# Optimization experiments

Hardware: AMD Instinct MI355X
Metric: run time of the kernel (lower is better)

Reference implementation:

```python
import jax, jax.numpy as jnp
import numpy as np

B, LT, D, N, H = 16, 512, 1024, 4096, 16
LN_EPS = 1e-5


def setup_inputs() -> dict:
    key = jax.random.key(0)
    ks = jax.random.split(key, 10)
    s = 0.02
    struct_token = jax.random.normal(ks[0], (N, D), dtype=jnp.float32)
    text_token = jax.random.normal(ks[1], (B, LT, D), dtype=jnp.float32)
    # contiguous, sorted segment ids: 256 struct tokens per batch element
    struct_batch = jnp.repeat(jnp.arange(B, dtype=jnp.int32), N // B)
    return {
        "struct_token": struct_token,
        "text_token": text_token,
        "in_proj_w": jax.random.normal(ks[2], (3 * D, D), dtype=jnp.float32) * s,
        "in_proj_b": jnp.zeros((3 * D,), jnp.float32),
        "attn_out_w": jax.random.normal(ks[3], (D, D), dtype=jnp.float32) * s,
        "attn_out_b": jnp.zeros((D,), jnp.float32),
        "ln_g": jnp.ones((D,), jnp.float32),
        "ln_b": jnp.zeros((D,), jnp.float32),
        "proj_w": jax.random.normal(ks[4], (D, D), dtype=jnp.float32) * s,
        "proj_b": jnp.zeros((D,), jnp.float32),
        "struct_batch": struct_batch,
        "L_max": N // B,
    }


def reference(struct_token, text_token, in_proj_w, in_proj_b, attn_out_w,
              attn_out_b, ln_g, ln_b, proj_w, proj_b, struct_batch, L_max):
    Bq = text_token.shape[0]
    Dm = struct_token.shape[-1]
    dh = Dm // H
    Ntok = struct_token.shape[0]

    # ---- ragged pad-pack (struct_batch is sorted/contiguous per segment) ----
    counts = jnp.bincount(struct_batch, length=Bq)                 # [B]
    starts = jnp.concatenate([jnp.zeros((1,), counts.dtype),
                              jnp.cumsum(counts)[:-1]])            # [B]
    pos = jnp.arange(Ntok) - starts[struct_batch]                  # [N] position in segment
    padded = jnp.zeros((Bq, L_max, Dm), struct_token.dtype)
    padded = padded.at[struct_batch, pos].set(struct_token)        # [B, Ls, D]

    # ---- nn.MultiheadAttention (batch_first): Q=padded, K=V=text ----
    wq, wk, wv = in_proj_w[:Dm], in_proj_w[Dm:2 * Dm], in_proj_w[2 * Dm:]
    bq, bk, bv = in_proj_b[:Dm], in_proj_b[Dm:2 * Dm], in_proj_b[2 * Dm:]
    q = (padded @ wq.T + bq).reshape(Bq, L_max, H, dh)
    k = (text_token @ wk.T + bk).reshape(Bq, -1, H, dh)
    v = (text_token @ wv.T + bv).reshape(Bq, -1, H, dh)
    scores = jnp.einsum('bqhd,bkhd->bhqk', q, k) / jnp.sqrt(jnp.float32(dh))
    attn = jax.nn.softmax(scores, axis=-1)
    ctx = jnp.einsum('bhqk,bkhd->bqhd', attn, v).reshape(Bq, L_max, Dm)
    fused = ctx @ attn_out_w.T + attn_out_b                        # [B, Ls, D]

    # ---- LayerNorm + output projection ----
    mu = fused.mean(-1, keepdims=True)
    var = fused.var(-1, keepdims=True)
    fused = (fused - mu) * jax.lax.rsqrt(var + LN_EPS) * ln_g + ln_b
    fused = fused @ proj_w.T + proj_b

    # ---- unpack valid tokens + scatter-mean over segments ----
    tok = fused[struct_batch, pos]                                 # [N, D]
    seg_sum = jax.ops.segment_sum(tok, struct_batch, num_segments=Bq)
    return seg_sum / jnp.maximum(counts, 1)[:, None].astype(seg_sum.dtype)
```

## Files before the change

kernel.cpp:

```cpp
#include <hip/hip_runtime.h>

constexpr int B  = 16;
constexpr int LT = 512;
constexpr int D  = 1024;
constexpr int N  = 4096;
constexpr int H  = 16;
constexpr int DH = D / H;
constexpr int LMAX = N / B;
constexpr float LN_EPS = 1e-5f;

typedef short  s16x8 __attribute__((ext_vector_type(8)));
typedef float  f32x4 __attribute__((ext_vector_type(4)));

__device__ __forceinline__ unsigned short f2bf(float x) {
    unsigned int u = __float_as_uint(x);
    unsigned int r = (u + 0x7fffu + ((u >> 16) & 1u)) >> 16;
    return (unsigned short)r;
}
__device__ __forceinline__ float bf2f(unsigned short u) {
    return __uint_as_float((unsigned int)u << 16);
}

__device__ __forceinline__ void load_lds16(const void* g, void* l) {
    __builtin_amdgcn_global_load_lds(
        (const __attribute__((address_space(1))) unsigned int*)g,
        (__attribute__((address_space(3))) unsigned int*)l, 16, 0, 0);
}

__global__ __launch_bounds__(256) void cast3_prep(
        const float* __restrict__ x0, unsigned short* __restrict__ y0, int n0,
        const float* __restrict__ x1, unsigned short* __restrict__ y1, int n1,
        const float* __restrict__ x2, unsigned short* __restrict__ y2, int n2,
        const int* __restrict__ sb, int* __restrict__ counts, int* __restrict__ starts,
        float* __restrict__ msum) {
    __shared__ int s_counts[B];
    int t = threadIdx.x;
    if (blockIdx.x == 6144) {
        if (t < B) s_counts[t] = 0;
        __syncthreads();
        for (int i = t; i < N; i += 256) atomicAdd(&s_counts[sb[i]], 1);
        __syncthreads();
        if (t == 0) {
            int run = 0;
            for (int b = 0; b < B; b++) { starts[b] = run; run += s_counts[b]; }
        }
        if (t < B) counts[t] = s_counts[t];
        return;
    }
    if (blockIdx.x == 6145) {
        float4 z = {0.f, 0.f, 0.f, 0.f};
#pragma unroll
        for (int c = 0; c < 16; c++)
            ((float4*)msum)[c * 256 + t] = z;
        return;
    }
    long long i = (long long)(blockIdx.x * 256 + t) * 8;
    const float* x; unsigned short* y;
    if (i < n0)                { x = x0 + i; y = y0 + i; }
    else if (i < (long long)n0 + n1) { long long j = i - n0; x = x1 + j; y = y1 + j; }
    else if (i < (long long)n0 + n1 + n2) { long long j = i - n0 - n1; x = x2 + j; y = y2 + j; }
    else return;
    float4 a = *(const float4*)x;
    float4 b = *(const float4*)(x + 4);
    ushort4 o1, o2;
    o1.x = f2bf(a.x); o1.y = f2bf(a.y); o1.z = f2bf(a.z); o1.w = f2bf(a.w);
    o2.x = f2bf(b.x); o2.y = f2bf(b.y); o2.z = f2bf(b.z); o2.w = f2bf(b.w);
    *(ushort4*)y = o1;
    *(ushort4*)(y + 4) = o2;
}

__global__ void scatter_full(const float* __restrict__ st,
                             const int* __restrict__ counts,
                             const int* __restrict__ starts,
                             unsigned short* __restrict__ padded) {
    int p = blockIdx.x, b = blockIdx.y;
    int d = threadIdx.x * 4;
    size_t off = ((size_t)(b * LMAX + p)) * D + d;
    ushort4 o = {0, 0, 0, 0};
    if (p < counts[b]) {
        float4 v = *(const float4*)&st[(size_t)(starts[b] + p) * D + d];
        o.x = f2bf(v.x); o.y = f2bf(v.y); o.z = f2bf(v.z); o.w = f2bf(v.w);
    }
    *(ushort4*)&padded[off] = o;
}

template<typename Epi>
__device__ __forceinline__ void gemm32(const unsigned short* __restrict__ A,
                                       const unsigned short* __restrict__ W,
                                       int K, int kbeg, int kend, int m0, int n0,
                                       unsigned short* __restrict__ As,
                                       unsigned short* __restrict__ Bs,
                                       Epi&& epi) {
    const int tid  = threadIdx.x;
    const int lane = tid & 63;
    const int wid  = tid >> 6;
    const int wr   = wid >> 1;
    const int wc   = wid & 1;
    const int fm   = lane & 15;
    const int quad = lane >> 4;
    const int NK   = (kend - kbeg) >> 5;

    f32x4 acc[4][4];
#pragma unroll
    for (int i = 0; i < 4; i++)
#pragma unroll
        for (int j = 0; j < 4; j++) acc[i][j] = (f32x4){0.f, 0.f, 0.f, 0.f};

    const int rA0 = tid >> 2,          sA0 = (tid & 3) ^ ((tid >> 3) & 3);
    const int cA1 = tid + 512;
    const int rA1 = cA1 >> 2,          sA1 = (cA1 & 3) ^ ((cA1 >> 3) & 3);
    const unsigned short* gA0 = A + (size_t)(m0 + rA0) * K + kbeg + sA0 * 8;
    const unsigned short* gA1 = A + (size_t)(m0 + rA1) * K + kbeg + sA1 * 8;
    const unsigned short* gB  = W + (size_t)(n0 + rA0) * K + kbeg + sA0 * 8;
    unsigned short* lA0 = As + (size_t)tid * 8;
    unsigned short* lA1 = As + (size_t)(tid + 512) * 8;
    unsigned short* lB  = Bs + (size_t)tid * 8;

    const int sl8 = (quad ^ ((fm >> 1) & 3)) * 8;
    int offA[4], offB[4];
#pragma unroll
    for (int i = 0; i < 4; i++) offA[i] = (wr * 64 + i * 16 + fm) * 32 + sl8;
#pragma unroll
    for (int j = 0; j < 4; j++) offB[j] = (wc * 64 + j * 16 + fm) * 32 + sl8;

    load_lds16(gA0, lA0);
    load_lds16(gA1, lA1);
    load_lds16(gB , lB );

    for (int s = 0; s < NK; s++) {
        const int ab = (s & 1) << 13;
        const int bb = (s & 1) << 12;
        asm volatile("s_barrier" ::: "memory");
        if (s + 1 < NK) {
            const int go = (s + 1) << 5;
            const int ab2 = ((s + 1) & 1) << 13;
            const int bb2 = ((s + 1) & 1) << 12;
            load_lds16(gA0 + go, lA0 + ab2);
            load_lds16(gA1 + go, lA1 + ab2);
            load_lds16(gB  + go, lB  + bb2);
            asm volatile("s_waitcnt vmcnt(3)" ::: "memory");
        } else {
            asm volatile("s_waitcnt vmcnt(0)" ::: "memory");
        }
        asm volatile("s_barrier" ::: "memory");

        s16x8 af[4], bfv[4];
#pragma unroll
        for (int i = 0; i < 4; i++) af[i] = *(const s16x8*)&As[ab + offA[i]];
#pragma unroll
        for (int j = 0; j < 4; j++) bfv[j] = *(const s16x8*)&Bs[bb + offB[j]];

        __builtin_amdgcn_s_setprio(1);
#pragma unroll
        for (int i = 0; i < 4; i++)
#pragma unroll
            for (int j = 0; j < 4; j++)
                acc[i][j] = __builtin_amdgcn_mfma_f32_16x16x32_bf16(af[i], bfv[j], acc[i][j], 0, 0, 0);
        __builtin_amdgcn_s_setprio(0);
    }

    const int fr = quad * 4;
#pragma unroll
    for (int i = 0; i < 4; i++)
#pragma unroll
        for (int j = 0; j < 4; j++) {
            int row = m0 + wr * 64 + i * 16 + fr;
            int col = n0 + wc * 64 + j * 16 + fm;
#pragma unroll
            for (int r = 0; r < 4; r++)
                epi(row + r, col, acc[i][j][r]);
        }
}

template<typename Epi>
__device__ __forceinline__ void gemm128(const unsigned short* __restrict__ A,
                                        const unsigned short* __restrict__ W,
                                        int K, int kbeg, int kend, int m0, int n0,
                                        unsigned short* __restrict__ As,
                                        unsigned short* __restrict__ Bs,
                                        Epi&& epi) {
    const int tid  = threadIdx.x;
    const int lane = tid & 63;
    const int wid  = tid >> 6;
    const int wr   = wid >> 1;
    const int wc   = wid & 1;
    const int fm   = lane & 15;
    const int quad = lane >> 4;
    const int NK   = (kend - kbeg) >> 5;

    f32x4 acc[4][4];
#pragma unroll
    for (int i = 0; i < 4; i++)
#pragma unroll
        for (int j = 0; j < 4; j++) acc[i][j] = (f32x4){0.f, 0.f, 0.f, 0.f};

    const int r0 = tid >> 2, s0 = (tid & 3) ^ ((tid >> 3) & 3);
    const unsigned short* gA0 = A + (size_t)(m0 + r0) * K + kbeg + s0 * 8;
    const unsigned short* gA1 = gA0 + (size_t)64 * K;
    const unsigned short* gB0 = W + (size_t)(n0 + r0) * K + kbeg + s0 * 8;
    const unsigned short* gB1 = gB0 + (size_t)64 * K;
    unsigned short* lA0 = As + (size_t)tid * 8;
    unsigned short* lA1 = As + (size_t)(tid + 256) * 8;
    unsigned short* lB0 = Bs + (size_t)tid * 8;
    unsigned short* lB1 = Bs + (size_t)(tid + 256) * 8;

    const int sl8 = (quad ^ ((fm >> 1) & 3)) * 8;
    int offA[4], offB[4];
#pragma unroll
    for (int i = 0; i < 4; i++) offA[i] = (wr * 64 + i * 16 + fm) * 32 + sl8;
#pragma unroll
    for (int j = 0; j < 4; j++) offB[j] = (wc * 64 + j * 16 + fm) * 32 + sl8;

    load_lds16(gA0, lA0);
    load_lds16(gA1, lA1);
    load_lds16(gB0, lB0);
    load_lds16(gB1, lB1);

    for (int s = 0; s < NK; s++) {
        const int ab = (s & 1) << 12;
        const int bb = (s & 1) << 12;
        asm volatile("s_barrier" ::: "memory");
        if (s + 1 < NK) {
            const int go = (s + 1) << 5;
            const int nb = ((s + 1) & 1) << 12;
            load_lds16(gA0 + go, lA0 + nb);
            load_lds16(gA1 + go, lA1 + nb);
            load_lds16(gB0 + go, lB0 + nb);
            load_lds16(gB1 + go, lB1 + nb);
            asm volatile("s_waitcnt vmcnt(4)" ::: "memory");
        } else {
            asm volatile("s_waitcnt vmcnt(0)" ::: "memory");
        }
        asm volatile("s_barrier" ::: "memory");

        s16x8 af[4], bfv[4];
#pragma unroll
        for (int i = 0; i < 4; i++) af[i] = *(const s16x8*)&As[ab + offA[i]];
#pragma unroll
        for (int j = 0; j < 4; j++) bfv[j] = *(const s16x8*)&Bs[bb + offB[j]];

        __builtin_amdgcn_s_setprio(1);
#pragma unroll
        for (int i = 0; i < 4; i++)
#pragma unroll
            for (int j = 0; j < 4; j++)
                acc[i][j] = __builtin_amdgcn_mfma_f32_16x16x32_bf16(af[i], bfv[j], acc[i][j], 0, 0, 0);
        __builtin_amdgcn_s_setprio(0);
    }

    const int fr = quad * 4;
#pragma unroll
    for (int i = 0; i < 4; i++)
#pragma unroll
        for (int j = 0; j < 4; j++) {
            int row = m0 + wr * 64 + i * 16 + fr;
            int col = n0 + wc * 64 + j * 16 + fm;
#pragma unroll
            for (int r = 0; r < 4; r++)
                epi(row + r, col, acc[i][j][r]);
        }
}

__global__ __launch_bounds__(512, 4) void qkv_fused(const unsigned short* __restrict__ padded,
                                                    const unsigned short* __restrict__ text,
                                                    const unsigned short* __restrict__ wqkv,
                                                    const float* __restrict__ bqkv,
                                                    unsigned short* __restrict__ qpack,
                                                    unsigned short* __restrict__ kpack,
                                                    unsigned short* __restrict__ vpack) {
    __shared__ __align__(16) unsigned short As[2 * 8192];
    __shared__ __align__(16) unsigned short Bs[2 * 4096];
    int orig = blockIdx.x;
    int id = (orig & 7) * 80 + (orig >> 3);
    if (id < 128) {
        int mt = id >> 3, nt = id & 7;
        gemm32(padded, wqkv, D, 0, D, mt * 256, nt * 128, As, Bs,
            [&](int mm, int col, float v) {
                float val = v + bqkv[col];
                int b = mm >> 8, q = mm & 255;
                int h = col >> 6, d = col & 63;
                qpack[(size_t)(b * H + h) * 16384 + (d >> 3) * 2048 + q * 8 + (d & 7)] = f2bf(val);
            });
    } else if (id < 384) {
        int f = id - 128;
        int mt = f >> 3, nt = f & 7;
        gemm32(text, wqkv + (size_t)D * D, D, 0, D, mt * 256, nt * 128, As, Bs,
            [&](int mm, int col, float v) {
                float val = v + bqkv[D + col];
                int b = mm >> 9, key = mm & 511;
                int h = col >> 6, d = col & 63;
                kpack[(size_t)(b * H + h) * 32768 + (d >> 3) * 4096 + key * 8 + (d & 7)] = f2bf(val);
            });
    } else {
        int f = id - 384;
        int mt = f >> 6, nt = f & 63;
        gemm32(wqkv + 2 * (size_t)D * D, text, D, 0, D, mt * 256, nt * 128, As, Bs,
            [&](int mm, int col, float v) {
                float val = v + bqkv[2 * D + mm];
                int h = mm >> 6, d = mm & 63;
                int b = col >> 9, key = col & 511;
                vpack[(size_t)(b * H + h) * 32768 + (key >> 3) * 512 + d * 8 + (key & 7)] = f2bf(val);
            });
    }
}

__global__ __launch_bounds__(256, 4) void gemm_bf2(const unsigned short* __restrict__ A,
                                                   const unsigned short* __restrict__ W,
                                                   unsigned short* __restrict__ C0,
                                                   unsigned short* __restrict__ C1,
                                                   int Nn, int K) {
    __shared__ __align__(16) unsigned short As[2 * 4096];
    __shared__ __align__(16) unsigned short Bs[2 * 4096];
    int orig = blockIdx.x;
    int id = (orig & 7) * 64 + (orig >> 3);
    int kh = id >> 8;
    int f  = id & 255;
    int mt = f >> 3, nt = f & 7;
    unsigned short* C = kh ? C1 : C0;
    gemm128(A, W, K, kh * 512, (kh + 1) * 512, mt * 128, nt * 128, As, Bs,
        [&](int mm, int col, float v) {
            C[(size_t)mm * Nn + col] = f2bf(v);
        });
}

constexpr int PKW = 72;

__global__ __launch_bounds__(512) void attn_mfma(const unsigned short* __restrict__ qpack,
                                                 const unsigned short* __restrict__ kpack,
                                                 const unsigned short* __restrict__ vpack,
                                                 unsigned short* __restrict__ ctx) {
    __shared__ __align__(16) unsigned short KV[2][16384];
    __shared__ __align__(16) unsigned short Ps[8 * 16 * PKW];

    const int tid = threadIdx.x;
    const int lane = tid & 63;
    const int wv = tid >> 6;
    const int fm = lane & 15;
    const int quad = lane >> 4;
    const int h = blockIdx.x, b = blockIdx.y, half = blockIdx.z;
    const int q0 = half * 128 + wv * 16;

    const unsigned short* qp = qpack + (size_t)(b * H + h) * 16384;
    const unsigned short* kp = kpack + (size_t)(b * H + h) * 32768;
    const unsigned short* vp = vpack + (size_t)(b * H + h) * 32768;

    const s16x8 aq0 = *(const s16x8*)&qp[quad * 2048 + (q0 + fm) * 8];
    const s16x8 aq1 = *(const s16x8*)&qp[(4 + quad) * 2048 + (q0 + fm) * 8];

#pragma unroll
    for (int kc = 0; kc < 2; kc++)
#pragma unroll
        for (int it = 0; it < 4; it++) {
            int f = it * 512 + tid;
            load_lds16(kp + (f >> 8) * 4096 + kc * 2048 + (f & 255) * 8, &KV[kc][f * 8]);
        }

    f32x4 sc[32];

    asm volatile("s_waitcnt vmcnt(4)" ::: "memory");
    __builtin_amdgcn_s_barrier();
    __builtin_amdgcn_s_setprio(1);
#pragma unroll
    for (int t = 0; t < 16; t++) {
        s16x8 bk0 = *(const s16x8*)&KV[0][quad * 2048 + (t * 16 + fm) * 8];
        s16x8 bk1 = *(const s16x8*)&KV[0][(4 + quad) * 2048 + (t * 16 + fm) * 8];
        f32x4 a = (f32x4){0.f, 0.f, 0.f, 0.f};
        a = __builtin_amdgcn_mfma_f32_16x16x32_bf16(aq0, bk0, a, 0, 0, 0);
        a = __builtin_amdgcn_mfma_f32_16x16x32_bf16(aq1, bk1, a, 0, 0, 0);
        sc[t] = a;
    }
    __builtin_amdgcn_s_setprio(0);

    asm volatile("s_waitcnt vmcnt(0)" ::: "memory");
    __builtin_amdgcn_s_barrier();
    __builtin_amdgcn_s_setprio(1);
#pragma unroll
    for (int t = 0; t < 16; t++) {
        s16x8 bk0 = *(const s16x8*)&KV[1][quad * 2048 + (t * 16 + fm) * 8];
        s16x8 bk1 = *(const s16x8*)&KV[1][(4 + quad) * 2048 + (t * 16 + fm) * 8];
        f32x4 a = (f32x4){0.f, 0.f, 0.f, 0.f};
        a = __builtin_amdgcn_mfma_f32_16x16x32_bf16(aq0, bk0, a, 0, 0, 0);
        a = __builtin_amdgcn_mfma_f32_16x16x32_bf16(aq1, bk1, a, 0, 0, 0);
        sc[16 + t] = a;
    }
    __builtin_amdgcn_s_setprio(0);

    asm volatile("s_waitcnt lgkmcnt(0)" ::: "memory");
    __builtin_amdgcn_s_barrier();

#pragma unroll
    for (int vc = 0; vc < 2; vc++)
#pragma unroll
        for (int it = 0; it < 4; it++) {
            int f = it * 512 + tid;
            load_lds16(vp + vc * 16384 + f * 8, &KV[vc][f * 8]);
        }

    const float scale = 0.125f;
    float mx[4], l[4], inv[4];
#pragma unroll
    for (int r = 0; r < 4; r++) {
        float m = sc[0][r];
#pragma unroll
        for (int t = 1; t < 32; t++) m = fmaxf(m, sc[t][r]);
        mx[r] = m;
    }
#pragma unroll
    for (int o = 1; o < 16; o <<= 1)
#pragma unroll
        for (int r = 0; r < 4; r++) mx[r] = fmaxf(mx[r], __shfl_xor(mx[r], o));
#pragma unroll
    for (int r = 0; r < 4; r++) l[r] = 0.f;
#pragma unroll
    for (int t = 0; t < 32; t++)
#pragma unroll
        for (int r = 0; r < 4; r++) {
            float e = __expf((sc[t][r] - mx[r]) * scale);
            sc[t][r] = e;
            l[r] += e;
        }
#pragma unroll
    for (int o = 1; o < 16; o <<= 1)
#pragma unroll
        for (int r = 0; r < 4; r++) l[r] += __shfl_xor(l[r], o);
#pragma unroll
    for (int r = 0; r < 4; r++) inv[r] = 1.f / l[r];

    f32x4 co[4];
#pragma unroll
    for (int n = 0; n < 4; n++) co[n] = (f32x4){0.f, 0.f, 0.f, 0.f};
    unsigned short* Pw = Ps + wv * (16 * PKW);

    asm volatile("s_waitcnt vmcnt(4)" ::: "memory");
    __builtin_amdgcn_s_barrier();

    for (int vc = 0; vc < 2; vc++) {
        if (vc == 1) {
            asm volatile("s_waitcnt vmcnt(0)" ::: "memory");
            __builtin_amdgcn_s_barrier();
        }
        for (int cs = 0; cs < 4; cs++) {
            int c = vc * 4 + cs;
#pragma unroll
            for (int tt = 0; tt < 4; tt++)
#pragma unroll
                for (int r = 0; r < 4; r++)
                    Pw[(quad * 4 + r) * PKW + tt * 16 + fm] = f2bf(sc[c * 4 + tt][r]);
            __builtin_amdgcn_s_setprio(1);
#pragma unroll
            for (int s = 0; s < 2; s++) {
                s16x8 ap = *(const s16x8*)&Pw[fm * PKW + s * 32 + quad * 8];
#pragma unroll
                for (int n = 0; n < 4; n++) {
                    s16x8 bv = *(const s16x8*)&KV[vc][(cs * 8 + s * 4 + quad) * 512 + (n * 16 + fm) * 8];
                    co[n] = __builtin_amdgcn_mfma_f32_16x16x32_bf16(ap, bv, co[n], 0, 0, 0);
                }
            }
            __builtin_amdgcn_s_setprio(0);
        }
    }

    const size_t obase = (size_t)(b * LMAX + q0) * D + h * DH;
#pragma unroll
    for (int n = 0; n < 4; n++)
#pragma unroll
        for (int r = 0; r < 4; r++)
            ctx[obase + (size_t)(quad * 4 + r) * D + n * 16 + fm] = f2bf(co[n][r] * inv[r]);
}

__global__ __launch_bounds__(256) void lnmean_kernel(const unsigned short* __restrict__ f1a,
                                                     const unsigned short* __restrict__ f1b,
                                                     const float* __restrict__ bo,
                                                     const float* __restrict__ g,
                                                     const float* __restrict__ bb,
                                                     const int* __restrict__ counts,
                                                     float* __restrict__ msum) {
    int b = blockIdx.x;
    int t = threadIdx.x;
    int wv = t >> 6, lane = t & 63;
    int cnt = counts[b];
    int s0 = blockIdx.y * 32 + wv * 8;
    int s1 = min(cnt, s0 + 8);

    float4 gg[4], bv[4], bo4[4];
#pragma unroll
    for (int c = 0; c < 4; c++) {
        gg[c]  = *(const float4*)&g[c * 256 + lane * 4];
        bv[c]  = *(const float4*)&bb[c * 256 + lane * 4];
        bo4[c] = *(const float4*)&bo[c * 256 + lane * 4];
    }
    float4 acc[4];
#pragma unroll
    for (int c = 0; c < 4; c++) acc[c] = (float4){0.f, 0.f, 0.f, 0.f};

    for (int s = s0; s < s1; s++) {
        size_t rbase = ((size_t)(b * LMAX + s)) * D;
        float4 v[4];
        float sm = 0.f, ss = 0.f;
#pragma unroll
        for (int c = 0; c < 4; c++) {
            ushort4 ua = *(const ushort4*)&f1a[rbase + c * 256 + lane * 4];
            ushort4 ub = *(const ushort4*)&f1b[rbase + c * 256 + lane * 4];
            v[c].x = bf2f(ua.x) + bf2f(ub.x) + bo4[c].x;
            v[c].y = bf2f(ua.y) + bf2f(ub.y) + bo4[c].y;
            v[c].z = bf2f(ua.z) + bf2f(ub.z) + bo4[c].z;
            v[c].w = bf2f(ua.w) + bf2f(ub.w) + bo4[c].w;
            sm += v[c].x + v[c].y + v[c].z + v[c].w;
            ss += v[c].x * v[c].x + v[c].y * v[c].y + v[c].z * v[c].z + v[c].w * v[c].w;
        }
#pragma unroll
        for (int o = 32; o; o >>= 1) { sm += __shfl_xor(sm, o); ss += __shfl_xor(ss, o); }
        float mu = sm * (1.f / D);
        float var = ss * (1.f / D) - mu * mu;
        float r = rsqrtf(var + LN_EPS);
#pragma unroll
        for (int c = 0; c < 4; c++) {
            acc[c].x += (v[c].x - mu) * r * gg[c].x + bv[c].x;
            acc[c].y += (v[c].y - mu) * r * gg[c].y + bv[c].y;
            acc[c].z += (v[c].z - mu) * r * gg[c].z + bv[c].z;
            acc[c].w += (v[c].w - mu) * r * gg[c].w + bv[c].w;
        }
    }
    float inv = 1.f / (float)max(cnt, 1);
#pragma unroll
    for (int c = 0; c < 4; c++) {
        int base = b * D + c * 256 + lane * 4;
        atomicAdd(&msum[base + 0], acc[c].x * inv);
        atomicAdd(&msum[base + 1], acc[c].y * inv);
        atomicAdd(&msum[base + 2], acc[c].z * inv);
        atomicAdd(&msum[base + 3], acc[c].w * inv);
    }
}

__global__ __launch_bounds__(256) void tproj_kernel(const float* __restrict__ msum,
                                                    const float* __restrict__ W,
                                                    const float* __restrict__ bias,
                                                    float* __restrict__ out) {
    int lane = threadIdx.x & 63;
    int n = blockIdx.x * 4 + (threadIdx.x >> 6);
    float4 wr[4];
#pragma unroll
    for (int i = 0; i < 4; i++)
        wr[i] = *(const float4*)&W[(size_t)n * D + i * 256 + lane * 4];
    float bn = bias[n];
    for (int b = 0; b < B; b++) {
        float s = 0.f;
#pragma unroll
        for (int i = 0; i < 4; i++) {
            float4 m4 = *(const float4*)&msum[(size_t)b * D + i * 256 + lane * 4];
            s += m4.x * wr[i].x + m4.y * wr[i].y + m4.z * wr[i].z + m4.w * wr[i].w;
        }
#pragma unroll
        for (int o = 32; o; o >>= 1) s += __shfl_xor(s, o);
        if (lane == 0) out[(size_t)b * D + n] = s + bn;
    }
}

extern "C" void kernel_launch(void* const* d_in, const int* in_sizes, int n_in,
                              void* d_out, int out_size, void* d_ws, size_t ws_size,
                              hipStream_t stream) {
    const float* struct_token = (const float*)d_in[0];
    const float* text_token   = (const float*)d_in[1];
    const float* in_proj_w    = (const float*)d_in[2];
    const float* in_proj_b    = (const float*)d_in[3];
    const float* attn_out_w   = (const float*)d_in[4];
    const float* attn_out_b   = (const float*)d_in[5];
    const float* ln_g         = (const float*)d_in[6];
    const float* ln_b         = (const float*)d_in[7];
    const float* proj_w       = (const float*)d_in[8];
    const float* proj_b       = (const float*)d_in[9];
    const int*   sb           = (const int*)d_in[10];
    float* out = (float*)d_out;

    const size_t MQ  = (size_t)B * LMAX;
    const size_t MKV = (size_t)B * LT;

    char* p = (char*)d_ws;
    unsigned short* padded_b = (unsigned short*)p;  p += MQ * D * 2;
    unsigned short* text_b   = (unsigned short*)p;  p += MKV * D * 2;
    unsigned short* wqkv_b   = (unsigned short*)p;  p += (size_t)3 * D * D * 2;
    unsigned short* wattn_b  = (unsigned short*)p;  p += (size_t)D * D * 2;
    unsigned short* qpack    = (unsigned short*)p;  p += MQ * D * 2;
    unsigned short* kpack    = (unsigned short*)p;  p += MKV * D * 2;
    unsigned short* vpack    = (unsigned short*)p;  p += MKV * D * 2;
    unsigned short* ctx_b    = (unsigned short*)p;  p += MQ * D * 2;
    unsigned short* f1a      = (unsigned short*)p;  p += MQ * D * 2;
    unsigned short* f1b      = (unsigned short*)p;  p += MQ * D * 2;
    float* msum = (float*)p;  p += (size_t)B * D * 4;
    int* counts = (int*)p;  p += B * 4;
    int* starts = (int*)p;  p += B * 4;

    cast3_prep<<<6146, 256, 0, stream>>>(
        text_token, text_b, (int)(MKV * D),
        in_proj_w,  wqkv_b, 3 * D * D,
        attn_out_w, wattn_b, D * D,
        sb, counts, starts, msum);

    scatter_full<<<dim3(LMAX, B), 256, 0, stream>>>(struct_token, counts, starts, padded_b);

    qkv_fused<<<640, 512, 0, stream>>>(padded_b, text_b, wqkv_b, in_proj_b,
                                       qpack, kpack, vpack);

    attn_mfma<<<dim3(H, B, 2), 512, 0, stream>>>(qpack, kpack, vpack, ctx_b);

    gemm_bf2<<<512, 256, 0, stream>>>(ctx_b, wattn_b, f1a, f1b, D, D);

    lnmean_kernel<<<dim3(B, 8), 256, 0, stream>>>(f1a, f1b, attn_out_b, ln_g, ln_b, counts, msum);

    tproj_kernel<<<256, 256, 0, stream>>>(msum, proj_w, proj_b, out);
}
```

Before: 253.8 us.

## Stream attention with online softmax over 128-key chunks and triple-buffered K/V

Rewrites the attention kernel as a flash-style online softmax over four 128-key chunks instead of holding all 512 scores in registers. K and V chunks rotate through a three-slot LDS ring (48KB instead of 64KB), and the next chunk is prefetched while the current one is computed. Launch bounds now request 4 blocks per CU. Both changes aim to cut register and LDS pressure so more waves fit per CU. The cost is extra rescaling work per chunk and more barriers.

```diff
diff --git a/kernel.cpp b/kernel.cpp
--- a/kernel.cpp
+++ b/kernel.cpp
@@ -325,11 +325,11 @@
 
 constexpr int PKW = 72;
 
-__global__ __launch_bounds__(512) void attn_mfma(const unsigned short* __restrict__ qpack,
-                                                 const unsigned short* __restrict__ kpack,
-                                                 const unsigned short* __restrict__ vpack,
-                                                 unsigned short* __restrict__ ctx) {
-    __shared__ __align__(16) unsigned short KV[2][16384];
+__global__ __launch_bounds__(512, 4) void attn_mfma(const unsigned short* __restrict__ qpack,
+                                                    const unsigned short* __restrict__ kpack,
+                                                    const unsigned short* __restrict__ vpack,
+                                                    unsigned short* __restrict__ ctx) {
+    __shared__ __align__(16) unsigned short KV[3][8192];
     __shared__ __align__(16) unsigned short Ps[8 * 16 * PKW];
 
     const int tid = threadIdx.x;
@@ -347,118 +347,130 @@
     const s16x8 aq0 = *(const s16x8*)&qp[quad * 2048 + (q0 + fm) * 8];
     const s16x8 aq1 = *(const s16x8*)&qp[(4 + quad) * 2048 + (q0 + fm) * 8];
 
-#pragma unroll
-    for (int kc = 0; kc < 2; kc++)
-#pragma unroll
-        for (int it = 0; it < 4; it++) {
+    auto stageK = [&](int c, int bfi) {
+#pragma unroll
+        for (int it = 0; it < 2; it++) {
             int f = it * 512 + tid;
-            load_lds16(kp + (f >> 8) * 4096 + kc * 2048 + (f & 255) * 8, &KV[kc][f * 8]);
-        }
-
-    f32x4 sc[32];
-
-    asm volatile("s_waitcnt vmcnt(4)" ::: "memory");
-    __builtin_amdgcn_s_barrier();
-    __builtin_amdgcn_s_setprio(1);
-#pragma unroll
-    for (int t = 0; t < 16; t++) {
-        s16x8 bk0 = *(const s16x8*)&KV[0][quad * 2048 + (t * 16 + fm) * 8];
-        s16x8 bk1 = *(const s16x8*)&KV[0][(4 + quad) * 2048 + (t * 16 + fm) * 8];
-        f32x4 a = (f32x4){0.f, 0.f, 0.f, 0.f};
-        a = __builtin_amdgcn_mfma_f32_16x16x32_bf16(aq0, bk0, a, 0, 0, 0);
-        a = __builtin_amdgcn_mfma_f32_16x16x32_bf16(aq1, bk1, a, 0, 0, 0);
-        sc[t] = a;
-    }
-    __builtin_amdgcn_s_setprio(0);
-
-    asm volatile("s_waitcnt vmcnt(0)" ::: "memory");
-    __builtin_amdgcn_s_barrier();
-    __builtin_amdgcn_s_setprio(1);
-#pragma unroll
-    for (int t = 0; t < 16; t++) {
-        s16x8 bk0 = *(const s16x8*)&KV[1][quad * 2048 + (t * 16 + fm) * 8];
-        s16x8 bk1 = *(const s16x8*)&KV[1][(4 + quad) * 2048 + (t * 16 + fm) * 8];
-        f32x4 a = (f32x4){0.f, 0.f, 0.f, 0.f};
-        a = __builtin_amdgcn_mfma_f32_16x16x32_bf16(aq0, bk0, a, 0, 0, 0);
-        a = __builtin_amdgcn_mfma_f32_16x16x32_bf16(aq1, bk1, a, 0, 0, 0);
-        sc[16 + t] = a;
-    }
-    __builtin_amdgcn_s_setprio(0);
-
-    asm volatile("s_waitcnt lgkmcnt(0)" ::: "memory");
-    __builtin_amdgcn_s_barrier();
-
-#pragma unroll
-    for (int vc = 0; vc < 2; vc++)
-#pragma unroll
-        for (int it = 0; it < 4; it++) {
+            load_lds16(kp + (f >> 7) * 4096 + c * 1024 + (f & 127) * 8, &KV[bfi][f * 8]);
+        }
+    };
+    auto stageV = [&](int c, int bfi) {
+#pragma unroll
+        for (int it = 0; it < 2; it++) {
             int f = it * 512 + tid;
-            load_lds16(vp + vc * 16384 + f * 8, &KV[vc][f * 8]);
-        }
+            load_lds16(vp + c * 8192 + f * 8, &KV[bfi][f * 8]);
+        }
+    };
 
     const float scale = 0.125f;
-    float mx[4], l[4], inv[4];
-#pragma unroll
-    for (int r = 0; r < 4; r++) {
-        float m = sc[0][r];
-#pragma unroll
-        for (int t = 1; t < 32; t++) m = fmaxf(m, sc[t][r]);
-        mx[r] = m;
-    }
-#pragma unroll
-    for (int o = 1; o < 16; o <<= 1)
-#pragma unroll
-        for (int r = 0; r < 4; r++) mx[r] = fmaxf(mx[r], __shfl_xor(mx[r], o));
-#pragma unroll
-    for (int r = 0; r < 4; r++) l[r] = 0.f;
-#pragma unroll
-    for (int t = 0; t < 32; t++)
+    f32x4 co[4];
+#pragma unroll
+    for (int n = 0; n < 4; n++) co[n] = (f32x4){0.f, 0.f, 0.f, 0.f};
+    float m[4], l[4];
+#pragma unroll
+    for (int r = 0; r < 4; r++) { m[r] = -1e30f; l[r] = 0.f; }
+
+    unsigned short* Pw = Ps + wv * (16 * PKW);
+
+    stageK(0, 0);
+    stageV(0, 1);
+
+#pragma unroll
+    for (int c = 0; c < 4; c++) {
+        const int kb = (2 * c) % 3;
+        const int vb = (2 * c + 1) % 3;
+
+        asm volatile("s_waitcnt vmcnt(2)" ::: "memory");
+        __builtin_amdgcn_s_barrier();
+
+        f32x4 sc[8];
+        __builtin_amdgcn_s_setprio(1);
+#pragma unroll
+        for (int t = 0; t < 8; t++) {
+            s16x8 bk0 = *(const s16x8*)&KV[kb][quad * 1024 + (t * 16 + fm) * 8];
+            s16x8 bk1 = *(const s16x8*)&KV[kb][(4 + quad) * 1024 + (t * 16 + fm) * 8];
+            f32x4 a = (f32x4){0.f, 0.f, 0.f, 0.f};
+            a = __builtin_amdgcn_mfma_f32_16x16x32_bf16(aq0, bk0, a, 0, 0, 0);
+            a = __builtin_amdgcn_mfma_f32_16x16x32_bf16(aq1, bk1, a, 0, 0, 0);
+            sc[t] = a;
+        }
+        __builtin_amdgcn_s_setprio(0);
+
+        asm volatile("s_waitcnt lgkmcnt(0)" ::: "memory");
+        __builtin_amdgcn_s_barrier();
+        if (c < 3) stageK(c + 1, (2 * c + 2) % 3);
+
+        float cm[4];
 #pragma unroll
         for (int r = 0; r < 4; r++) {
-            float e = __expf((sc[t][r] - mx[r]) * scale);
-            sc[t][r] = e;
-            l[r] += e;
-        }
-#pragma unroll
-    for (int o = 1; o < 16; o <<= 1)
-#pragma unroll
-        for (int r = 0; r < 4; r++) l[r] += __shfl_xor(l[r], o);
-#pragma unroll
-    for (int r = 0; r < 4; r++) inv[r] = 1.f / l[r];
-
-    f32x4 co[4];
-#pragma unroll
-    for (int n = 0; n < 4; n++) co[n] = (f32x4){0.f, 0.f, 0.f, 0.f};
-    unsigned short* Pw = Ps + wv * (16 * PKW);
-
-    asm volatile("s_waitcnt vmcnt(4)" ::: "memory");
-    __builtin_amdgcn_s_barrier();
-
-    for (int vc = 0; vc < 2; vc++) {
-        if (vc == 1) {
-            asm volatile("s_waitcnt vmcnt(0)" ::: "memory");
-            __builtin_amdgcn_s_barrier();
-        }
-        for (int cs = 0; cs < 4; cs++) {
-            int c = vc * 4 + cs;
+            float mm = sc[0][r];
+#pragma unroll
+            for (int t = 1; t < 8; t++) mm = fmaxf(mm, sc[t][r]);
+            cm[r] = mm;
+        }
+#pragma unroll
+        for (int o = 1; o < 16; o <<= 1)
+#pragma unroll
+            for (int r = 0; r < 4; r++) cm[r] = fmaxf(cm[r], __shfl_xor(cm[r], o));
+        float al[4];
+#pragma unroll
+        for (int r = 0; r < 4; r++) {
+            float mn = fmaxf(m[r], cm[r]);
+            al[r] = __expf((m[r] - mn) * scale);
+            m[r] = mn;
+        }
+        float ls[4] = {0.f, 0.f, 0.f, 0.f};
+#pragma unroll
+        for (int t = 0; t < 8; t++)
+#pragma unroll
+            for (int r = 0; r < 4; r++) {
+                float e = __expf((sc[t][r] - m[r]) * scale);
+                sc[t][r] = e;
+                ls[r] += e;
+            }
+#pragma unroll
+        for (int r = 0; r < 4; r++) l[r] = l[r] * al[r] + ls[r];
+#pragma unroll
+        for (int n = 0; n < 4; n++)
+#pragma unroll
+            for (int r = 0; r < 4; r++) co[n][r] *= al[r];
+
+        if (c < 3) asm volatile("s_waitcnt vmcnt(2)" ::: "memory");
+        else       asm volatile("s_waitcnt vmcnt(0)" ::: "memory");
+        __builtin_amdgcn_s_barrier();
+
+#pragma unroll
+        for (int cs = 0; cs < 2; cs++) {
 #pragma unroll
             for (int tt = 0; tt < 4; tt++)
 #pragma unroll
                 for (int r = 0; r < 4; r++)
-                    Pw[(quad * 4 + r) * PKW + tt * 16 + fm] = f2bf(sc[c * 4 + tt][r]);
+                    Pw[(quad * 4 + r) * PKW + tt * 16 + fm] = f2bf(sc[cs * 4 + tt][r]);
             __builtin_amdgcn_s_setprio(1);
 #pragma unroll
             for (int s = 0; s < 2; s++) {
                 s16x8 ap = *(const s16x8*)&Pw[fm * PKW + s * 32 + quad * 8];
 #pragma unroll
                 for (int n = 0; n < 4; n++) {
-                    s16x8 bv = *(const s16x8*)&KV[vc][(cs * 8 + s * 4 + quad) * 512 + (n * 16 + fm) * 8];
+                    s16x8 bv = *(const s16x8*)&KV[vb][(cs * 8 + s * 4 + quad) * 512 + (n * 16 + fm) * 8];
                     co[n] = __builtin_amdgcn_mfma_f32_16x16x32_bf16(ap, bv, co[n], 0, 0, 0);
                 }
             }
             __builtin_amdgcn_s_setprio(0);
         }
-    }
+
+        asm volatile("s_waitcnt lgkmcnt(0)" ::: "memory");
+        __builtin_amdgcn_s_barrier();
+        if (c < 3) stageV(c + 1, (2 * c + 3) % 3);
+    }
+
+    float inv[4];
+#pragma unroll
+    for (int o = 1; o < 16; o <<= 1)
+#pragma unroll
+        for (int r = 0; r < 4; r++) l[r] += __shfl_xor(l[r], o);
+#pragma unroll
+    for (int r = 0; r < 4; r++) inv[r] = 1.f / l[r];
 
     const size_t obase = (size_t)(b * LMAX + q0) * D + h * DH;
 #pragma unroll
```

New measurement: 282.2 us. +11.2%, slower.

## Retile QKV GEMM to 128x128 tiles with K-step 64 and 256 threads

Applied to the files above, without the earlier changes.

The fused QKV projection kernel moves from 256x128 output tiles with 512 threads and a K-step of 32 to 128x128 tiles with 256 threads and a K-step of 64. Grid size doubles to 1280 blocks. The LDS swizzle is changed to an 8-way XOR layout, and each stage issues 8 async loads per thread with a matching vmcnt wait. The goal is fewer barriers per unit of MFMA work and better load balance across CUs. In exchange, each tile reuses less data, so global traffic per FLOP rises, and LDS grows to 64KB per block.

```diff
diff --git a/kernel.cpp b/kernel.cpp
--- a/kernel.cpp
+++ b/kernel.cpp
@@ -85,12 +85,12 @@
 }
 
 template<typename Epi>
-__device__ __forceinline__ void gemm32(const unsigned short* __restrict__ A,
-                                       const unsigned short* __restrict__ W,
-                                       int K, int kbeg, int kend, int m0, int n0,
-                                       unsigned short* __restrict__ As,
-                                       unsigned short* __restrict__ Bs,
-                                       Epi&& epi) {
+__device__ __forceinline__ void gemm128k64(const unsigned short* __restrict__ A,
+                                           const unsigned short* __restrict__ W,
+                                           int K, int kbeg, int kend, int m0, int n0,
+                                           unsigned short* __restrict__ As,
+                                           unsigned short* __restrict__ Bs,
+                                           Epi&& epi) {
     const int tid  = threadIdx.x;
     const int lane = tid & 63;
     const int wid  = tid >> 6;
@@ -98,7 +98,7 @@
     const int wc   = wid & 1;
     const int fm   = lane & 15;
     const int quad = lane >> 4;
-    const int NK   = (kend - kbeg) >> 5;
+    const int NK   = (kend - kbeg) >> 6;
 
     f32x4 acc[4][4];
 #pragma unroll
@@ -106,56 +106,73 @@
 #pragma unroll
         for (int j = 0; j < 4; j++) acc[i][j] = (f32x4){0.f, 0.f, 0.f, 0.f};
 
-    const int rA0 = tid >> 2,          sA0 = (tid & 3) ^ ((tid >> 3) & 3);
-    const int cA1 = tid + 512;
-    const int rA1 = cA1 >> 2,          sA1 = (cA1 & 3) ^ ((cA1 >> 3) & 3);
-    const unsigned short* gA0 = A + (size_t)(m0 + rA0) * K + kbeg + sA0 * 8;
-    const unsigned short* gA1 = A + (size_t)(m0 + rA1) * K + kbeg + sA1 * 8;
-    const unsigned short* gB  = W + (size_t)(n0 + rA0) * K + kbeg + sA0 * 8;
-    unsigned short* lA0 = As + (size_t)tid * 8;
-    unsigned short* lA1 = As + (size_t)(tid + 512) * 8;
-    unsigned short* lB  = Bs + (size_t)tid * 8;
-
-    const int sl8 = (quad ^ ((fm >> 1) & 3)) * 8;
-    int offA[4], offB[4];
-#pragma unroll
-    for (int i = 0; i < 4; i++) offA[i] = (wr * 64 + i * 16 + fm) * 32 + sl8;
-#pragma unroll
-    for (int j = 0; j < 4; j++) offB[j] = (wc * 64 + j * 16 + fm) * 32 + sl8;
-
-    load_lds16(gA0, lA0);
-    load_lds16(gA1, lA1);
-    load_lds16(gB , lB );
+    int rows[4], go8[4];
+#pragma unroll
+    for (int k = 0; k < 4; k++) {
+        int ci = tid + k * 256;
+        rows[k] = ci >> 3;
+        go8[k]  = ((ci & 7) ^ ((ci >> 3) & 7)) * 8;
+    }
+    const unsigned short* gA[4];
+    const unsigned short* gB[4];
+#pragma unroll
+    for (int k = 0; k < 4; k++) {
+        gA[k] = A + (size_t)(m0 + rows[k]) * K + kbeg + go8[k];
+        gB[k] = W + (size_t)(n0 + rows[k]) * K + kbeg + go8[k];
+    }
+
+    auto stage = [&](int s) {
+        const int go = s << 6;
+        unsigned short* Ad = As + (s & 1) * 8192;
+        unsigned short* Bd = Bs + (s & 1) * 8192;
+#pragma unroll
+        for (int k = 0; k < 4; k++)
+            load_lds16(gA[k] + go, Ad + (size_t)(tid + k * 256) * 8);
+#pragma unroll
+        for (int k = 0; k < 4; k++)
+            load_lds16(gB[k] + go, Bd + (size_t)(tid + k * 256) * 8);
+    };
+
+    int offA[4][2], offB[4][2];
+#pragma unroll
+    for (int kk = 0; kk < 2; kk++) {
+        const int sl8 = ((kk * 4 + quad) ^ (fm & 7)) * 8;
+#pragma unroll
+        for (int i = 0; i < 4; i++) offA[i][kk] = (wr * 64 + i * 16 + fm) * 64 + sl8;
+#pragma unroll
+        for (int j = 0; j < 4; j++) offB[j][kk] = (wc * 64 + j * 16 + fm) * 64 + sl8;
+    }
+
+    stage(0);
 
     for (int s = 0; s < NK; s++) {
         const int ab = (s & 1) << 13;
-        const int bb = (s & 1) << 12;
         asm volatile("s_barrier" ::: "memory");
         if (s + 1 < NK) {
-            const int go = (s + 1) << 5;
-            const int ab2 = ((s + 1) & 1) << 13;
-            const int bb2 = ((s + 1) & 1) << 12;
-            load_lds16(gA0 + go, lA0 + ab2);
-            load_lds16(gA1 + go, lA1 + ab2);
-            load_lds16(gB  + go, lB  + bb2);
-            asm volatile("s_waitcnt vmcnt(3)" ::: "memory");
+            stage(s + 1);
+            asm volatile("s_waitcnt vmcnt(8)" ::: "memory");
         } else {
             asm volatile("s_waitcnt vmcnt(0)" ::: "memory");
         }
         asm volatile("s_barrier" ::: "memory");
 
-        s16x8 af[4], bfv[4];
-#pragma unroll
-        for (int i = 0; i < 4; i++) af[i] = *(const s16x8*)&As[ab + offA[i]];
-#pragma unroll
-        for (int j = 0; j < 4; j++) bfv[j] = *(const s16x8*)&Bs[bb + offB[j]];
+        s16x8 af[4][2], bfv[4][2];
+#pragma unroll
+        for (int kk = 0; kk < 2; kk++) {
+#pragma unroll
+            for (int i = 0; i < 4; i++) af[i][kk]  = *(const s16x8*)&As[ab + offA[i][kk]];
+#pragma unroll
+            for (int j = 0; j < 4; j++) bfv[j][kk] = *(const s16x8*)&Bs[ab + offB[j][kk]];
+        }
 
         __builtin_amdgcn_s_setprio(1);
 #pragma unroll
-        for (int i = 0; i < 4; i++)
-#pragma unroll
-            for (int j = 0; j < 4; j++)
-                acc[i][j] = __builtin_amdgcn_mfma_f32_16x16x32_bf16(af[i], bfv[j], acc[i][j], 0, 0, 0);
+        for (int kk = 0; kk < 2; kk++)
+#pragma unroll
+            for (int i = 0; i < 4; i++)
+#pragma unroll
+                for (int j = 0; j < 4; j++)
+                    acc[i][j] = __builtin_amdgcn_mfma_f32_16x16x32_bf16(af[i][kk], bfv[j][kk], acc[i][j], 0, 0, 0);
         __builtin_amdgcn_s_setprio(0);
     }
 
@@ -261,7 +278,7 @@
         }
 }
 
-__global__ __launch_bounds__(512, 4) void qkv_fused(const unsigned short* __restrict__ padded,
+__global__ __launch_bounds__(256, 2) void qkv_fused(const unsigned short* __restrict__ padded,
                                                     const unsigned short* __restrict__ text,
                                                     const unsigned short* __restrict__ wqkv,
                                                     const float* __restrict__ bqkv,
@@ -269,22 +286,22 @@
                                                     unsigned short* __restrict__ kpack,
                                                     unsigned short* __restrict__ vpack) {
     __shared__ __align__(16) unsigned short As[2 * 8192];
-    __shared__ __align__(16) unsigned short Bs[2 * 4096];
+    __shared__ __align__(16) unsigned short Bs[2 * 8192];
     int orig = blockIdx.x;
-    int id = (orig & 7) * 80 + (orig >> 3);
-    if (id < 128) {
+    int id = (orig & 7) * 160 + (orig >> 3);
+    if (id < 256) {
         int mt = id >> 3, nt = id & 7;
-        gemm32(padded, wqkv, D, 0, D, mt * 256, nt * 128, As, Bs,
+        gemm128k64(padded, wqkv, D, 0, D, mt * 128, nt * 128, As, Bs,
             [&](int mm, int col, float v) {
                 float val = v + bqkv[col];
                 int b = mm >> 8, q = mm & 255;
                 int h = col >> 6, d = col & 63;
                 qpack[(size_t)(b * H + h) * 16384 + (d >> 3) * 2048 + q * 8 + (d & 7)] = f2bf(val);
             });
-    } else if (id < 384) {
-        int f = id - 128;
+    } else if (id < 768) {
+        int f = id - 256;
         int mt = f >> 3, nt = f & 7;
-        gemm32(text, wqkv + (size_t)D * D, D, 0, D, mt * 256, nt * 128, As, Bs,
+        gemm128k64(text, wqkv + (size_t)D * D, D, 0, D, mt * 128, nt * 128, As, Bs,
             [&](int mm, int col, float v) {
                 float val = v + bqkv[D + col];
                 int b = mm >> 9, key = mm & 511;
@@ -292,9 +309,9 @@
                 kpack[(size_t)(b * H + h) * 32768 + (d >> 3) * 4096 + key * 8 + (d & 7)] = f2bf(val);
             });
     } else {
-        int f = id - 384;
+        int f = id - 768;
         int mt = f >> 6, nt = f & 63;
-        gemm32(wqkv + 2 * (size_t)D * D, text, D, 0, D, mt * 256, nt * 128, As, Bs,
+        gemm128k64(wqkv + 2 * (size_t)D * D, text, D, 0, D, mt * 128, nt * 128, As, Bs,
             [&](int mm, int col, float v) {
                 float val = v + bqkv[2 * D + mm];
                 int h = mm >> 6, d = mm & 63;
@@ -598,8 +615,8 @@
 
     scatter_full<<<dim3(LMAX, B), 256, 0, stream>>>(struct_token, counts, starts, padded_b);
 
-    qkv_fused<<<640, 512, 0, stream>>>(padded_b, text_b, wqkv_b, in_proj_b,
-                                       qpack, kpack, vpack);
+    qkv_fused<<<1280, 256, 0, stream>>>(padded_b, text_b, wqkv_b, in_proj_b,
+                                        qpack, kpack, vpack);
 
     attn_mfma<<<dim3(H, B, 2), 512, 0, stream>>>(qpack, kpack, vpack, ctx_b);
 
```

Measured after the change: 252.8 us. No clear change (-0.4%).
